# Kernel optimization log

Hardware: AMD Instinct MI355X
Metric: run time of the kernel (lower is better)

Reference implementation:

```python
import jax, jax.numpy as jnp
import numpy as np

N_NODES = 20000
N_EDGES = 640000
HIDDEN = 128


def setup_inputs() -> dict:
    key = jax.random.key(0)
    k1, k2, k3, k4 = jax.random.split(key, 4)
    scale = 1.0 / np.sqrt(HIDDEN)
    features = jax.random.normal(k1, (N_NODES, HIDDEN), dtype=jnp.float32)
    edge_index = jax.random.randint(k2, (2, N_EDGES), 0, N_NODES, dtype=jnp.int64)
    W_l = jax.random.normal(k3, (HIDDEN, HIDDEN), dtype=jnp.float32) * scale
    b_l = jnp.zeros((HIDDEN,), dtype=jnp.float32)
    W_r = jax.random.normal(k4, (HIDDEN, HIDDEN), dtype=jnp.float32) * scale
    return {"features": features, "edge_index": edge_index, "W_l": W_l, "b_l": b_l, "W_r": W_r}


def reference(features, edge_index, W_l, b_l, W_r):
    # PyG SAGEConv with mean aggregation:
    #   out_i = lin_l(mean_{j : (j->i) in E} x_j) + lin_r(x_i)
    # edge_index[0] = source nodes, edge_index[1] = target nodes.
    n = features.shape[0]
    src = edge_index[0]
    dst = edge_index[1]
    msg = features[src]  # [E, d] gather
    summed = jax.ops.segment_sum(msg, dst, num_segments=n)  # [N, d] scatter-add
    cnt = jax.ops.segment_sum(jnp.ones(src.shape[0], dtype=features.dtype), dst, num_segments=n)
    agg = summed / jnp.maximum(cnt, 1.0)[:, None]  # mean; isolated nodes -> 0
    return agg @ W_l.T + b_l + features @ W_r.T
```

## Files before the change

kernel.cpp:

```cpp
#include <hip/hip_runtime.h>

#define N_NODES 20000
#define N_EDGES 640000
#define HIDDEN  128
#define CAP     96
#define DEG_PAD 16

typedef unsigned short bf16_t;
typedef __attribute__((ext_vector_type(8))) short short8;
typedef __attribute__((ext_vector_type(8))) unsigned short ushort8_t;
typedef __attribute__((ext_vector_type(4))) float floatx4;

__device__ __forceinline__ bf16_t f2bf(float f) {
    union { float f; unsigned int i; } v; v.f = f;
    unsigned int x = v.i + 0x7FFFu + ((v.i >> 16) & 1u);
    return (bf16_t)(x >> 16);
}
__device__ __forceinline__ float bflo(unsigned u) {
    union { unsigned i; float f; } v; v.i = u << 16; return v.f;
}
__device__ __forceinline__ float bfhi(unsigned u) {
    union { unsigned i; float f; } v; v.i = u & 0xFFFF0000u; return v.f;
}

__global__ __launch_bounds__(256) void prep_fill_kernel(
        const float* __restrict__ feat,
        const float* __restrict__ Wl,
        const float* __restrict__ Wr,
        const int* __restrict__ eidx,
        bf16_t* __restrict__ feat_bf,
        bf16_t* __restrict__ Bp,
        int* __restrict__ deg,
        unsigned short* __restrict__ bucket) {
    int t = blockIdx.x * 256 + threadIdx.x;
    float4 v = ((const float4*)feat)[t];
    ushort4 o = { f2bf(v.x), f2bf(v.y), f2bf(v.z), f2bf(v.w) };
    ((ushort4*)feat_bf)[t] = o;
    int src = eidx[t];
    int dst = eidx[N_EDGES + t];
    int pos = atomicAdd(&deg[dst * DEG_PAD], 1);
    if (pos < CAP) bucket[dst * CAP + pos] = (unsigned short)src;
    if (t < 2 * HIDDEN * HIDDEN) {
        int j    = t & 7;
        int lane = (t >> 3) & 63;
        int nt   = (t >> 9) & 15;
        int kt   = t >> 13;
        int n = nt * 16 + (lane & 15);
        int k = kt * 32 + (lane >> 4) * 8 + j;
        float w = (n < HIDDEN) ? Wl[n * HIDDEN + k] : Wr[(n - HIDDEN) * HIDDEN + k];
        Bp[t] = f2bf(w);
    }
}

__global__ __launch_bounds__(256) void gemm_kernel(
        const bf16_t* __restrict__ feat_bf,
        const bf16_t* __restrict__ Bp,
        const float* __restrict__ bl,
        bf16_t* __restrict__ Y,
        float* __restrict__ Z) {
    int wid = blockIdx.x * 4 + (threadIdx.x >> 6);
    if (wid >= N_NODES / 16) return;
    int lane = threadIdx.x & 63;
    int m    = lane & 15;
    int quad = lane >> 4;
    int row0 = wid * 16;

    floatx4 acc[16];
    floatx4 zf = {0.f, 0.f, 0.f, 0.f};
#pragma unroll
    for (int nt = 0; nt < 16; ++nt) acc[nt] = zf;

    const short8* bp = (const short8*)Bp;
#pragma unroll
    for (int kt = 0; kt < 4; ++kt) {
        short8 afrag = *(const short8*)(feat_bf + (size_t)(row0 + m) * HIDDEN
                                        + kt * 32 + quad * 8);
#pragma unroll
        for (int nt = 0; nt < 16; ++nt) {
            short8 bfrag = bp[(kt * 16 + nt) * 64 + lane];
            acc[nt] = __builtin_amdgcn_mfma_f32_16x16x32_bf16(afrag, bfrag, acc[nt], 0, 0, 0);
        }
    }
    int col = lane & 15;
#pragma unroll
    for (int nt = 0; nt < 8; ++nt) {
#pragma unroll
        for (int r = 0; r < 4; ++r) {
            int row = row0 + quad * 4 + r;
            Y[(size_t)row * HIDDEN + nt * 16 + col] = f2bf(acc[nt][r]);
        }
    }
#pragma unroll
    for (int nt = 8; nt < 16; ++nt) {
        float b = bl[(nt - 8) * 16 + col];
#pragma unroll
        for (int r = 0; r < 4; ++r) {
            int row = row0 + quad * 4 + r;
            Z[(size_t)row * HIDDEN + (nt - 8) * 16 + col] = acc[nt][r] + b;
        }
    }
}

__global__ __launch_bounds__(256) void gather_final_kernel(
        const bf16_t* __restrict__ Y,
        const float* __restrict__ Z,
        const int* __restrict__ deg,
        const unsigned short* __restrict__ bucket,
        float* __restrict__ out) {
    int wid  = (blockIdx.x * 256 + threadIdx.x) >> 6;
    int lane = threadIdx.x & 63;
    if (wid >= N_NODES) return;
    int d_true = deg[wid * DEG_PAD];
    int d = min(d_true, CAP);
    const unsigned short* row = bucket + wid * CAP;
    const unsigned* y = (const unsigned*)Y;
    float ax0=0,ay0=0, ax1=0,ay1=0, ax2=0,ay2=0, ax3=0,ay3=0;
    int i = 0;
    for (; i + 8 <= d; i += 8) {
        ushort8_t s = *(const ushort8_t*)(row + i);
        unsigned u0 = y[(int)s[0] * 64 + lane];
        unsigned u1 = y[(int)s[1] * 64 + lane];
        unsigned u2 = y[(int)s[2] * 64 + lane];
        unsigned u3 = y[(int)s[3] * 64 + lane];
        unsigned u4 = y[(int)s[4] * 64 + lane];
        unsigned u5 = y[(int)s[5] * 64 + lane];
        unsigned u6 = y[(int)s[6] * 64 + lane];
        unsigned u7 = y[(int)s[7] * 64 + lane];
        ax0 += bflo(u0); ay0 += bfhi(u0);
        ax1 += bflo(u1); ay1 += bfhi(u1);
        ax2 += bflo(u2); ay2 += bfhi(u2);
        ax3 += bflo(u3); ay3 += bfhi(u3);
        ax0 += bflo(u4); ay0 += bfhi(u4);
        ax1 += bflo(u5); ay1 += bfhi(u5);
        ax2 += bflo(u6); ay2 += bfhi(u6);
        ax3 += bflo(u7); ay3 += bfhi(u7);
    }
    for (; i < d; ++i) {
        unsigned u = y[(int)row[i] * 64 + lane];
        ax0 += bflo(u); ay0 += bfhi(u);
    }
    float inv = 1.0f / fmaxf((float)d_true, 1.0f);
    float2 z = ((const float2*)Z)[wid * 64 + lane];
    float2 r;
    r.x = (ax0 + ax1 + ax2 + ax3) * inv + z.x;
    r.y = (ay0 + ay1 + ay2 + ay3) * inv + z.y;
    ((float2*)out)[wid * 64 + lane] = r;
}

extern "C" void kernel_launch(void* const* d_in, const int* in_sizes, int n_in,
                              void* d_out, int out_size, void* d_ws, size_t ws_size,
                              hipStream_t stream) {
    const float* feat = (const float*)d_in[0];
    const int*   eidx = (const int*)d_in[1];
    const float* Wl   = (const float*)d_in[2];
    const float* bl   = (const float*)d_in[3];
    const float* Wr   = (const float*)d_in[4];
    float* out = (float*)d_out;

    int*            deg     = (int*)d_ws;
    unsigned short* bucket  = (unsigned short*)(deg + N_NODES * DEG_PAD);
    bf16_t*         Bp      = (bf16_t*)(bucket + (size_t)N_NODES * CAP);
    bf16_t*         feat_bf = Bp + 2 * HIDDEN * HIDDEN;
    bf16_t*         Y       = feat_bf + (size_t)N_NODES * HIDDEN;
    float*          Z       = (float*)(Y + (size_t)N_NODES * HIDDEN);

    hipMemsetAsync(deg, 0, (size_t)N_NODES * DEG_PAD * sizeof(int), stream);

    prep_fill_kernel<<<N_EDGES / 256, 256, 0, stream>>>(
        feat, Wl, Wr, eidx, feat_bf, Bp, deg, bucket);
    gemm_kernel<<<(N_NODES / 16 + 3) / 4, 256, 0, stream>>>(feat_bf, Bp, bl, Y, Z);
    gather_final_kernel<<<(N_NODES * 64) / 256, 256, 0, stream>>>(Y, Z, deg, bucket, out);
}
```

Baseline: 136.3 us.

## Replicate degree counters and buckets across 8 block-indexed replicas

Splits the per-destination degree counter and neighbor bucket into 8 replicas chosen by block index, so concurrent atomics on the same destination are spread across separate counters instead of padded single counters. The gather kernel reads all 8 replica counts and each replica's first 8 indices up front, then sums across replicas. This is meant to cut atomic contention in the bucket fill. In exchange the gather does more small loads per node and uses a smaller per-replica cap of 32, which silently drops edges if a replica overflows.

```diff
diff --git a/kernel.cpp b/kernel.cpp
--- a/kernel.cpp
+++ b/kernel.cpp
@@ -3,8 +3,8 @@
 #define N_NODES 20000
 #define N_EDGES 640000
 #define HIDDEN  128
-#define CAP     96
-#define DEG_PAD 16
+#define NREP    8
+#define RCAP    32
 
 typedef unsigned short bf16_t;
 typedef __attribute__((ext_vector_type(8))) short short8;
@@ -33,13 +33,15 @@
         int* __restrict__ deg,
         unsigned short* __restrict__ bucket) {
     int t = blockIdx.x * 256 + threadIdx.x;
+    int rep = blockIdx.x & (NREP - 1);
     float4 v = ((const float4*)feat)[t];
     ushort4 o = { f2bf(v.x), f2bf(v.y), f2bf(v.z), f2bf(v.w) };
     ((ushort4*)feat_bf)[t] = o;
     int src = eidx[t];
     int dst = eidx[N_EDGES + t];
-    int pos = atomicAdd(&deg[dst * DEG_PAD], 1);
-    if (pos < CAP) bucket[dst * CAP + pos] = (unsigned short)src;
+    int pos = atomicAdd(&deg[rep * N_NODES + dst], 1);
+    if (pos < RCAP)
+        bucket[(size_t)(rep * N_NODES + dst) * RCAP + pos] = (unsigned short)src;
     if (t < 2 * HIDDEN * HIDDEN) {
         int j    = t & 7;
         int lane = (t >> 3) & 63;
@@ -110,41 +112,50 @@
     int wid  = (blockIdx.x * 256 + threadIdx.x) >> 6;
     int lane = threadIdx.x & 63;
     if (wid >= N_NODES) return;
-    int d_true = deg[wid * DEG_PAD];
-    int d = min(d_true, CAP);
-    const unsigned short* row = bucket + wid * CAP;
     const unsigned* y = (const unsigned*)Y;
+
+    int d[NREP];
+#pragma unroll
+    for (int r = 0; r < NREP; ++r) d[r] = deg[r * N_NODES + wid];
+    ushort8_t s[NREP];
+#pragma unroll
+    for (int r = 0; r < NREP; ++r)
+        s[r] = *(const ushort8_t*)(bucket + (size_t)(r * N_NODES + wid) * RCAP);
+
     float ax0=0,ay0=0, ax1=0,ay1=0, ax2=0,ay2=0, ax3=0,ay3=0;
-    int i = 0;
-    for (; i + 8 <= d; i += 8) {
-        ushort8_t s = *(const ushort8_t*)(row + i);
-        unsigned u0 = y[(int)s[0] * 64 + lane];
-        unsigned u1 = y[(int)s[1] * 64 + lane];
-        unsigned u2 = y[(int)s[2] * 64 + lane];
-        unsigned u3 = y[(int)s[3] * 64 + lane];
-        unsigned u4 = y[(int)s[4] * 64 + lane];
-        unsigned u5 = y[(int)s[5] * 64 + lane];
-        unsigned u6 = y[(int)s[6] * 64 + lane];
-        unsigned u7 = y[(int)s[7] * 64 + lane];
-        ax0 += bflo(u0); ay0 += bfhi(u0);
-        ax1 += bflo(u1); ay1 += bfhi(u1);
-        ax2 += bflo(u2); ay2 += bfhi(u2);
-        ax3 += bflo(u3); ay3 += bfhi(u3);
-        ax0 += bflo(u4); ay0 += bfhi(u4);
-        ax1 += bflo(u5); ay1 += bfhi(u5);
-        ax2 += bflo(u6); ay2 += bfhi(u6);
-        ax3 += bflo(u7); ay3 += bfhi(u7);
+    int total = 0;
+#pragma unroll
+    for (int r = 0; r < NREP; ++r) {
+        int dr = d[r];
+        total += dr;
+        int dc = min(dr, RCAP);
+        int n8 = min(dc, 8);
+#pragma unroll
+        for (int j = 0; j < 8; ++j) {
+            if (j < n8) {
+                unsigned u = y[(int)s[r][j] * 64 + lane];
+                switch (j & 3) {
+                    case 0: ax0 += bflo(u); ay0 += bfhi(u); break;
+                    case 1: ax1 += bflo(u); ay1 += bfhi(u); break;
+                    case 2: ax2 += bflo(u); ay2 += bfhi(u); break;
+                    default: ax3 += bflo(u); ay3 += bfhi(u); break;
+                }
+            }
+        }
+        if (dc > 8) {
+            const unsigned short* row = bucket + (size_t)(r * N_NODES + wid) * RCAP;
+            for (int j = 8; j < dc; ++j) {
+                unsigned u = y[(int)row[j] * 64 + lane];
+                ax0 += bflo(u); ay0 += bfhi(u);
+            }
+        }
     }
-    for (; i < d; ++i) {
-        unsigned u = y[(int)row[i] * 64 + lane];
-        ax0 += bflo(u); ay0 += bfhi(u);
-    }
-    float inv = 1.0f / fmaxf((float)d_true, 1.0f);
+    float inv = 1.0f / fmaxf((float)total, 1.0f);
     float2 z = ((const float2*)Z)[wid * 64 + lane];
-    float2 r;
-    r.x = (ax0 + ax1 + ax2 + ax3) * inv + z.x;
-    r.y = (ay0 + ay1 + ay2 + ay3) * inv + z.y;
-    ((float2*)out)[wid * 64 + lane] = r;
+    float2 rr;
+    rr.x = (ax0 + ax1 + ax2 + ax3) * inv + z.x;
+    rr.y = (ay0 + ay1 + ay2 + ay3) * inv + z.y;
+    ((float2*)out)[wid * 64 + lane] = rr;
 }
 
 extern "C" void kernel_launch(void* const* d_in, const int* in_sizes, int n_in,
@@ -158,13 +169,13 @@
     float* out = (float*)d_out;
 
     int*            deg     = (int*)d_ws;
-    unsigned short* bucket  = (unsigned short*)(deg + N_NODES * DEG_PAD);
-    bf16_t*         Bp      = (bf16_t*)(bucket + (size_t)N_NODES * CAP);
+    unsigned short* bucket  = (unsigned short*)(deg + NREP * N_NODES);
+    bf16_t*         Bp      = (bf16_t*)(bucket + (size_t)NREP * N_NODES * RCAP);
     bf16_t*         feat_bf = Bp + 2 * HIDDEN * HIDDEN;
     bf16_t*         Y       = feat_bf + (size_t)N_NODES * HIDDEN;
     float*          Z       = (float*)(Y + (size_t)N_NODES * HIDDEN);
 
-    hipMemsetAsync(deg, 0, (size_t)N_NODES * DEG_PAD * sizeof(int), stream);
+    hipMemsetAsync(deg, 0, (size_t)NREP * N_NODES * sizeof(int), stream);
 
     prep_fill_kernel<<<N_EDGES / 256, 256, 0, stream>>>(
         feat, Wl, Wr, eidx, feat_bf, Bp, deg, bucket);
```

New measurement: 150.3 us. +10.2%, slower.

## Fuse pipeline into cooperative persistent kernel with GEMM overlapped with bucket fill

Applied to the files above, without the earlier changes.

Replaces the memset plus three separate launches with a single cooperative persistent kernel of 512 blocks, using grid-wide syncs between phases. In the middle phase half the blocks run the GEMM tiles while the other half do the atomic degree count and bucket fill, so the two overlap. This removes launch gaps and the separate memset, at the cost of grid.sync overhead, reduced parallelism per phase, and a grid sized to fit co-residency. The original multi-kernel path is kept as a fallback if the cooperative launch fails.

```diff
diff --git a/kernel.cpp b/kernel.cpp
--- a/kernel.cpp
+++ b/kernel.cpp
@@ -1,10 +1,17 @@
 #include <hip/hip_runtime.h>
+#include <hip/hip_cooperative_groups.h>
+
+namespace cg = cooperative_groups;
 
 #define N_NODES 20000
 #define N_EDGES 640000
 #define HIDDEN  128
 #define CAP     96
 #define DEG_PAD 16
+#define NB      512
+#define GEMM_NB 256
+#define FILL_T  ((NB - GEMM_NB) * 256)
+#define N_TILES (N_NODES / 16)
 
 typedef unsigned short bf16_t;
 typedef __attribute__((ext_vector_type(8))) short short8;
@@ -23,23 +30,16 @@
     union { unsigned i; float f; } v; v.i = u & 0xFFFF0000u; return v.f;
 }
 
-__global__ __launch_bounds__(256) void prep_fill_kernel(
-        const float* __restrict__ feat,
-        const float* __restrict__ Wl,
-        const float* __restrict__ Wr,
-        const int* __restrict__ eidx,
-        bf16_t* __restrict__ feat_bf,
-        bf16_t* __restrict__ Bp,
-        int* __restrict__ deg,
-        unsigned short* __restrict__ bucket) {
-    int t = blockIdx.x * 256 + threadIdx.x;
-    float4 v = ((const float4*)feat)[t];
-    ushort4 o = { f2bf(v.x), f2bf(v.y), f2bf(v.z), f2bf(v.w) };
-    ((ushort4*)feat_bf)[t] = o;
-    int src = eidx[t];
-    int dst = eidx[N_EDGES + t];
-    int pos = atomicAdd(&deg[dst * DEG_PAD], 1);
-    if (pos < CAP) bucket[dst * CAP + pos] = (unsigned short)src;
+__device__ __forceinline__ void do_feat_cvt(const float* feat, bf16_t* feat_bf,
+                                            int start, int stride) {
+    for (int i = start; i < (N_NODES * HIDDEN) / 4; i += stride) {
+        float4 v = ((const float4*)feat)[i];
+        ushort4 o = { f2bf(v.x), f2bf(v.y), f2bf(v.z), f2bf(v.w) };
+        ((ushort4*)feat_bf)[i] = o;
+    }
+}
+__device__ __forceinline__ void do_bp_pack(const float* Wl, const float* Wr,
+                                           bf16_t* Bp, int t) {
     if (t < 2 * HIDDEN * HIDDEN) {
         int j    = t & 7;
         int lane = (t >> 3) & 63;
@@ -51,25 +51,16 @@
         Bp[t] = f2bf(w);
     }
 }
-
-__global__ __launch_bounds__(256) void gemm_kernel(
-        const bf16_t* __restrict__ feat_bf,
-        const bf16_t* __restrict__ Bp,
-        const float* __restrict__ bl,
-        bf16_t* __restrict__ Y,
-        float* __restrict__ Z) {
-    int wid = blockIdx.x * 4 + (threadIdx.x >> 6);
-    if (wid >= N_NODES / 16) return;
-    int lane = threadIdx.x & 63;
+__device__ __forceinline__ void do_gemm_tile(int wid, int lane,
+        const bf16_t* feat_bf, const bf16_t* Bp, const float* bl,
+        bf16_t* Y, float* Z) {
     int m    = lane & 15;
     int quad = lane >> 4;
     int row0 = wid * 16;
-
     floatx4 acc[16];
     floatx4 zf = {0.f, 0.f, 0.f, 0.f};
 #pragma unroll
     for (int nt = 0; nt < 16; ++nt) acc[nt] = zf;
-
     const short8* bp = (const short8*)Bp;
 #pragma unroll
     for (int kt = 0; kt < 4; ++kt) {
@@ -100,19 +91,12 @@
         }
     }
 }
-
-__global__ __launch_bounds__(256) void gather_final_kernel(
-        const bf16_t* __restrict__ Y,
-        const float* __restrict__ Z,
-        const int* __restrict__ deg,
-        const unsigned short* __restrict__ bucket,
-        float* __restrict__ out) {
-    int wid  = (blockIdx.x * 256 + threadIdx.x) >> 6;
-    int lane = threadIdx.x & 63;
-    if (wid >= N_NODES) return;
+__device__ __forceinline__ void do_gather_node(int wid, int lane,
+        const bf16_t* Y, const float* Z, const int* deg,
+        const unsigned short* bucket, float* out) {
     int d_true = deg[wid * DEG_PAD];
     int d = min(d_true, CAP);
-    const unsigned short* row = bucket + wid * CAP;
+    const unsigned short* row = bucket + (size_t)wid * CAP;
     const unsigned* y = (const unsigned*)Y;
     float ax0=0,ay0=0, ax1=0,ay1=0, ax2=0,ay2=0, ax3=0,ay3=0;
     int i = 0;
@@ -147,6 +131,86 @@
     ((float2*)out)[wid * 64 + lane] = r;
 }
 
+__global__ __launch_bounds__(256, 2) void mega_kernel(
+        const float* __restrict__ feat,
+        const int* __restrict__ eidx,
+        const float* __restrict__ Wl,
+        const float* __restrict__ bl,
+        const float* __restrict__ Wr,
+        bf16_t* __restrict__ feat_bf,
+        bf16_t* __restrict__ Bp,
+        int* __restrict__ deg,
+        unsigned short* __restrict__ bucket,
+        bf16_t* __restrict__ Y,
+        float* __restrict__ Z,
+        float* __restrict__ out) {
+    cg::grid_group grid = cg::this_grid();
+    const int gid = blockIdx.x * 256 + threadIdx.x;
+
+    for (int i = gid; i < (N_NODES * DEG_PAD) / 4; i += NB * 256) {
+        int4 zz = {0, 0, 0, 0};
+        ((int4*)deg)[i] = zz;
+    }
+    do_feat_cvt(feat, feat_bf, gid, NB * 256);
+    do_bp_pack(Wl, Wr, Bp, gid);
+    grid.sync();
+
+    if (blockIdx.x < GEMM_NB) {
+        int wv   = blockIdx.x * 4 + (threadIdx.x >> 6);
+        int lane = threadIdx.x & 63;
+        for (int wid = wv; wid < N_TILES; wid += GEMM_NB * 4)
+            do_gemm_tile(wid, lane, feat_bf, Bp, bl, Y, Z);
+    } else {
+        int tid = (blockIdx.x - GEMM_NB) * 256 + threadIdx.x;
+        for (int e = tid; e < N_EDGES; e += FILL_T) {
+            int src = eidx[e];
+            int dst = eidx[N_EDGES + e];
+            int pos = atomicAdd(&deg[dst * DEG_PAD], 1);
+            if (pos < CAP) bucket[dst * CAP + pos] = (unsigned short)src;
+        }
+    }
+    grid.sync();
+
+    int wv   = gid >> 6;
+    int lane = threadIdx.x & 63;
+    for (int wid = wv; wid < N_NODES; wid += (NB * 256) / 64)
+        do_gather_node(wid, lane, Y, Z, deg, bucket, out);
+}
+
+__global__ __launch_bounds__(256) void prep_fill_kernel(
+        const float* __restrict__ feat, const float* __restrict__ Wl,
+        const float* __restrict__ Wr, const int* __restrict__ eidx,
+        bf16_t* __restrict__ feat_bf, bf16_t* __restrict__ Bp,
+        int* __restrict__ deg, unsigned short* __restrict__ bucket) {
+    int t = blockIdx.x * 256 + threadIdx.x;
+    {
+        float4 v = ((const float4*)feat)[t];
+        ushort4 o = { f2bf(v.x), f2bf(v.y), f2bf(v.z), f2bf(v.w) };
+        ((ushort4*)feat_bf)[t] = o;
+    }
+    int src = eidx[t];
+    int dst = eidx[N_EDGES + t];
+    int pos = atomicAdd(&deg[dst * DEG_PAD], 1);
+    if (pos < CAP) bucket[dst * CAP + pos] = (unsigned short)src;
+    do_bp_pack(Wl, Wr, Bp, t);
+}
+__global__ __launch_bounds__(256) void gemm_kernel(
+        const bf16_t* __restrict__ feat_bf, const bf16_t* __restrict__ Bp,
+        const float* __restrict__ bl, bf16_t* __restrict__ Y,
+        float* __restrict__ Z) {
+    int wid = blockIdx.x * 4 + (threadIdx.x >> 6);
+    if (wid >= N_TILES) return;
+    do_gemm_tile(wid, threadIdx.x & 63, feat_bf, Bp, bl, Y, Z);
+}
+__global__ __launch_bounds__(256) void gather_final_kernel(
+        const bf16_t* __restrict__ Y, const float* __restrict__ Z,
+        const int* __restrict__ deg, const unsigned short* __restrict__ bucket,
+        float* __restrict__ out) {
+    int wid = (blockIdx.x * 256 + threadIdx.x) >> 6;
+    if (wid >= N_NODES) return;
+    do_gather_node(wid, threadIdx.x & 63, Y, Z, deg, bucket, out);
+}
+
 extern "C" void kernel_launch(void* const* d_in, const int* in_sizes, int n_in,
                               void* d_out, int out_size, void* d_ws, size_t ws_size,
                               hipStream_t stream) {
@@ -164,10 +228,17 @@
     bf16_t*         Y       = feat_bf + (size_t)N_NODES * HIDDEN;
     float*          Z       = (float*)(Y + (size_t)N_NODES * HIDDEN);
 
-    hipMemsetAsync(deg, 0, (size_t)N_NODES * DEG_PAD * sizeof(int), stream);
-
-    prep_fill_kernel<<<N_EDGES / 256, 256, 0, stream>>>(
-        feat, Wl, Wr, eidx, feat_bf, Bp, deg, bucket);
-    gemm_kernel<<<(N_NODES / 16 + 3) / 4, 256, 0, stream>>>(feat_bf, Bp, bl, Y, Z);
-    gather_final_kernel<<<(N_NODES * 64) / 256, 256, 0, stream>>>(Y, Z, deg, bucket, out);
-}
+    void* args[] = { (void*)&feat, (void*)&eidx, (void*)&Wl, (void*)&bl, (void*)&Wr,
+                     (void*)&feat_bf, (void*)&Bp, (void*)&deg, (void*)&bucket,
+                     (void*)&Y, (void*)&Z, (void*)&out };
+    hipError_t err = hipLaunchCooperativeKernel((void*)mega_kernel, dim3(NB),
+                                                dim3(256), args, 0, stream);
+    if (err != hipSuccess) {
+        hipMemsetAsync(deg, 0, (size_t)N_NODES * DEG_PAD * sizeof(int), stream);
+        prep_fill_kernel<<<N_EDGES / 256, 256, 0, stream>>>(
+            feat, Wl, Wr, eidx, feat_bf, Bp, deg, bucket);
+        gemm_kernel<<<(N_TILES + 3) / 4, 256, 0, stream>>>(feat_bf, Bp, bl, Y, Z);
+        gather_final_kernel<<<(N_NODES * 64) / 256, 256, 0, stream>>>(
+            Y, Z, deg, bucket, out);
+    }
+}
```

Measured after the change: 312.7 us. 2.29x slower.

## Fuse edge bucket fill into GEMM launch and zero degrees in prep kernel

Applied to the files above, without the earlier changes.

Removes the separate memset by zeroing degree counters inside the prep kernel. Moves the edge bucketing (atomic degree count and bucket write) out of prep and into the GEMM launch, with separate block ranges for GEMM tiles and edge fill so the two can run concurrently. It also adds a 16-wide unrolled gather loop for more loads in flight. The combined launch is meant to overlap the atomic-heavy fill with MFMA work and save a launch, at the cost of more register pressure in the gather loop.

```diff
diff --git a/kernel.cpp b/kernel.cpp
--- a/kernel.cpp
+++ b/kernel.cpp
@@ -5,6 +5,9 @@
 #define HIDDEN  128
 #define CAP     96
 #define DEG_PAD 16
+#define GEMM_NB 313
+#define FILL_NB 2500
+#define N_TILES (N_NODES / 16)
 
 typedef unsigned short bf16_t;
 typedef __attribute__((ext_vector_type(8))) short short8;
@@ -23,23 +26,20 @@
     union { unsigned i; float f; } v; v.i = u & 0xFFFF0000u; return v.f;
 }
 
-__global__ __launch_bounds__(256) void prep_fill_kernel(
+__global__ __launch_bounds__(256) void prep_kernel(
         const float* __restrict__ feat,
         const float* __restrict__ Wl,
         const float* __restrict__ Wr,
-        const int* __restrict__ eidx,
         bf16_t* __restrict__ feat_bf,
         bf16_t* __restrict__ Bp,
-        int* __restrict__ deg,
-        unsigned short* __restrict__ bucket) {
+        int* __restrict__ deg) {
     int t = blockIdx.x * 256 + threadIdx.x;
-    float4 v = ((const float4*)feat)[t];
-    ushort4 o = { f2bf(v.x), f2bf(v.y), f2bf(v.z), f2bf(v.w) };
-    ((ushort4*)feat_bf)[t] = o;
-    int src = eidx[t];
-    int dst = eidx[N_EDGES + t];
-    int pos = atomicAdd(&deg[dst * DEG_PAD], 1);
-    if (pos < CAP) bucket[dst * CAP + pos] = (unsigned short)src;
+    {
+        float4 v = ((const float4*)feat)[t];
+        ushort4 o = { f2bf(v.x), f2bf(v.y), f2bf(v.z), f2bf(v.w) };
+        ((ushort4*)feat_bf)[t] = o;
+    }
+    if (t < N_NODES) deg[t * DEG_PAD] = 0;
     if (t < 2 * HIDDEN * HIDDEN) {
         int j    = t & 7;
         int lane = (t >> 3) & 63;
@@ -52,52 +52,64 @@
     }
 }
 
-__global__ __launch_bounds__(256) void gemm_kernel(
+__global__ __launch_bounds__(256) void fill_gemm_kernel(
         const bf16_t* __restrict__ feat_bf,
         const bf16_t* __restrict__ Bp,
         const float* __restrict__ bl,
+        const int* __restrict__ eidx,
         bf16_t* __restrict__ Y,
-        float* __restrict__ Z) {
-    int wid = blockIdx.x * 4 + (threadIdx.x >> 6);
-    if (wid >= N_NODES / 16) return;
-    int lane = threadIdx.x & 63;
-    int m    = lane & 15;
-    int quad = lane >> 4;
-    int row0 = wid * 16;
-
-    floatx4 acc[16];
-    floatx4 zf = {0.f, 0.f, 0.f, 0.f};
-#pragma unroll
-    for (int nt = 0; nt < 16; ++nt) acc[nt] = zf;
-
-    const short8* bp = (const short8*)Bp;
-#pragma unroll
-    for (int kt = 0; kt < 4; ++kt) {
-        short8 afrag = *(const short8*)(feat_bf + (size_t)(row0 + m) * HIDDEN
-                                        + kt * 32 + quad * 8);
-#pragma unroll
-        for (int nt = 0; nt < 16; ++nt) {
-            short8 bfrag = bp[(kt * 16 + nt) * 64 + lane];
-            acc[nt] = __builtin_amdgcn_mfma_f32_16x16x32_bf16(afrag, bfrag, acc[nt], 0, 0, 0);
+        float* __restrict__ Z,
+        int* __restrict__ deg,
+        unsigned short* __restrict__ bucket) {
+    if (blockIdx.x < GEMM_NB) {
+        int wid = blockIdx.x * 4 + (threadIdx.x >> 6);
+        if (wid >= N_TILES) return;
+        int lane = threadIdx.x & 63;
+        int m    = lane & 15;
+        int quad = lane >> 4;
+        int row0 = wid * 16;
+
+        floatx4 acc[16];
+        floatx4 zf = {0.f, 0.f, 0.f, 0.f};
+#pragma unroll
+        for (int nt = 0; nt < 16; ++nt) acc[nt] = zf;
+
+        const short8* bp = (const short8*)Bp;
+#pragma unroll
+        for (int kt = 0; kt < 4; ++kt) {
+            short8 afrag = *(const short8*)(feat_bf + (size_t)(row0 + m) * HIDDEN
+                                            + kt * 32 + quad * 8);
+#pragma unroll
+            for (int nt = 0; nt < 16; ++nt) {
+                short8 bfrag = bp[(kt * 16 + nt) * 64 + lane];
+                acc[nt] = __builtin_amdgcn_mfma_f32_16x16x32_bf16(afrag, bfrag, acc[nt], 0, 0, 0);
+            }
         }
-    }
-    int col = lane & 15;
-#pragma unroll
-    for (int nt = 0; nt < 8; ++nt) {
-#pragma unroll
-        for (int r = 0; r < 4; ++r) {
-            int row = row0 + quad * 4 + r;
-            Y[(size_t)row * HIDDEN + nt * 16 + col] = f2bf(acc[nt][r]);
+        int col = lane & 15;
+#pragma unroll
+        for (int nt = 0; nt < 8; ++nt) {
+#pragma unroll
+            for (int r = 0; r < 4; ++r) {
+                int row = row0 + quad * 4 + r;
+                Y[(size_t)row * HIDDEN + nt * 16 + col] = f2bf(acc[nt][r]);
+            }
         }
-    }
-#pragma unroll
-    for (int nt = 8; nt < 16; ++nt) {
-        float b = bl[(nt - 8) * 16 + col];
-#pragma unroll
-        for (int r = 0; r < 4; ++r) {
-            int row = row0 + quad * 4 + r;
-            Z[(size_t)row * HIDDEN + (nt - 8) * 16 + col] = acc[nt][r] + b;
+#pragma unroll
+        for (int nt = 8; nt < 16; ++nt) {
+            float b = bl[(nt - 8) * 16 + col];
+#pragma unroll
+            for (int r = 0; r < 4; ++r) {
+                int row = row0 + quad * 4 + r;
+                Z[(size_t)row * HIDDEN + (nt - 8) * 16 + col] = acc[nt][r] + b;
+            }
         }
+    } else {
+        int e = (blockIdx.x - GEMM_NB) * 256 + threadIdx.x;
+        if (e >= N_EDGES) return;
+        int src = eidx[e];
+        int dst = eidx[N_EDGES + e];
+        int pos = atomicAdd(&deg[dst * DEG_PAD], 1);
+        if (pos < CAP) bucket[dst * CAP + pos] = (unsigned short)src;
     }
 }
 
@@ -112,10 +124,46 @@
     if (wid >= N_NODES) return;
     int d_true = deg[wid * DEG_PAD];
     int d = min(d_true, CAP);
-    const unsigned short* row = bucket + wid * CAP;
+    const unsigned short* row = bucket + (size_t)wid * CAP;
     const unsigned* y = (const unsigned*)Y;
     float ax0=0,ay0=0, ax1=0,ay1=0, ax2=0,ay2=0, ax3=0,ay3=0;
     int i = 0;
+    for (; i + 16 <= d; i += 16) {
+        ushort8_t s0 = *(const ushort8_t*)(row + i);
+        ushort8_t s1 = *(const ushort8_t*)(row + i + 8);
+        unsigned u0 = y[(int)s0[0] * 64 + lane];
+        unsigned u1 = y[(int)s0[1] * 64 + lane];
+        unsigned u2 = y[(int)s0[2] * 64 + lane];
+        unsigned u3 = y[(int)s0[3] * 64 + lane];
+        unsigned u4 = y[(int)s0[4] * 64 + lane];
+        unsigned u5 = y[(int)s0[5] * 64 + lane];
+        unsigned u6 = y[(int)s0[6] * 64 + lane];
+        unsigned u7 = y[(int)s0[7] * 64 + lane];
+        unsigned v0 = y[(int)s1[0] * 64 + lane];
+        unsigned v1 = y[(int)s1[1] * 64 + lane];
+        unsigned v2 = y[(int)s1[2] * 64 + lane];
+        unsigned v3 = y[(int)s1[3] * 64 + lane];
+        unsigned v4 = y[(int)s1[4] * 64 + lane];
+        unsigned v5 = y[(int)s1[5] * 64 + lane];
+        unsigned v6 = y[(int)s1[6] * 64 + lane];
+        unsigned v7 = y[(int)s1[7] * 64 + lane];
+        ax0 += bflo(u0); ay0 += bfhi(u0);
+        ax1 += bflo(u1); ay1 += bfhi(u1);
+        ax2 += bflo(u2); ay2 += bfhi(u2);
+        ax3 += bflo(u3); ay3 += bfhi(u3);
+        ax0 += bflo(u4); ay0 += bfhi(u4);
+        ax1 += bflo(u5); ay1 += bfhi(u5);
+        ax2 += bflo(u6); ay2 += bfhi(u6);
+        ax3 += bflo(u7); ay3 += bfhi(u7);
+        ax0 += bflo(v0); ay0 += bfhi(v0);
+        ax1 += bflo(v1); ay1 += bfhi(v1);
+        ax2 += bflo(v2); ay2 += bfhi(v2);
+        ax3 += bflo(v3); ay3 += bfhi(v3);
+        ax0 += bflo(v4); ay0 += bfhi(v4);
+        ax1 += bflo(v5); ay1 += bfhi(v5);
+        ax2 += bflo(v6); ay2 += bfhi(v6);
+        ax3 += bflo(v7); ay3 += bfhi(v7);
+    }
     for (; i + 8 <= d; i += 8) {
         ushort8_t s = *(const ushort8_t*)(row + i);
         unsigned u0 = y[(int)s[0] * 64 + lane];
@@ -164,10 +212,9 @@
     bf16_t*         Y       = feat_bf + (size_t)N_NODES * HIDDEN;
     float*          Z       = (float*)(Y + (size_t)N_NODES * HIDDEN);
 
-    hipMemsetAsync(deg, 0, (size_t)N_NODES * DEG_PAD * sizeof(int), stream);
-
-    prep_fill_kernel<<<N_EDGES / 256, 256, 0, stream>>>(
-        feat, Wl, Wr, eidx, feat_bf, Bp, deg, bucket);
-    gemm_kernel<<<(N_NODES / 16 + 3) / 4, 256, 0, stream>>>(feat_bf, Bp, bl, Y, Z);
-    gather_final_kernel<<<(N_NODES * 64) / 256, 256, 0, stream>>>(Y, Z, deg, bucket, out);
-}
+    prep_kernel<<<2500, 256, 0, stream>>>(feat, Wl, Wr, feat_bf, Bp, deg);
+    fill_gemm_kernel<<<GEMM_NB + FILL_NB, 256, 0, stream>>>(
+        feat_bf, Bp, bl, eidx, Y, Z, deg, bucket);
+    gather_final_kernel<<<(N_NODES * 64) / 256, 256, 0, stream>>>(
+        Y, Z, deg, bucket, out);
+}
```

After: 139.5 us. 2.4% more time.
